# Optimization experiments

Measured on AMD Instinct MI355X. Metric: run time of the kernel, lower is better.

Reference implementation:

```python
import jax, jax.numpy as jnp
import numpy as np

DIM = 512
NUM_HEADS = 16
WIN = (7, 7)
SIZE = WIN[0] * WIN[1]  # 49
B = 2048   # total windows
NW = 4     # windows per image (mask groups)


def _relative_position_index():
    coords_h = np.arange(WIN[0])
    coords_w = np.arange(WIN[1])
    coords = np.stack(np.meshgrid(coords_h, coords_w, indexing='ij'))  # [2,Wh,Ww]
    flat = coords.reshape(2, -1)                                       # [2,S]
    rel = flat[:, :, None] - flat[:, None, :]                          # [2,S,S]
    rel = rel.transpose(1, 2, 0)                                       # [S,S,2]
    rel[:, :, 0] += WIN[0] - 1
    rel[:, :, 1] += WIN[1] - 1
    rel[:, :, 0] *= 2 * WIN[1] - 1
    return rel.sum(-1).astype(np.int32)                                # [S,S]


def setup_inputs() -> dict:
    key = jax.random.key(0)
    ks = jax.random.split(key, 8)
    num_bias = (2 * WIN[0] - 1) * (2 * WIN[1] - 1)  # 169
    sd = 1.0 / np.sqrt(DIM)
    return {
        'x': jax.random.normal(ks[0], (B, SIZE, DIM), dtype=jnp.float32),
        'mask': jax.random.normal(ks[1], (NW, SIZE, SIZE), dtype=jnp.float32),
        'w_qkv': jax.random.normal(ks[2], (DIM, 3 * DIM), dtype=jnp.float32) * sd,
        'b_qkv': jnp.zeros((3 * DIM,), dtype=jnp.float32),
        'w_proj': jax.random.normal(ks[3], (DIM, DIM), dtype=jnp.float32) * sd,
        'b_proj': jnp.zeros((DIM,), dtype=jnp.float32),
        'bias_table': jax.random.normal(ks[4], (num_bias, NUM_HEADS), dtype=jnp.float32) * 0.02,
        'rel_idx': jnp.asarray(_relative_position_index()),
    }


def reference(x, mask, w_qkv, b_qkv, w_proj, b_proj, bias_table, rel_idx):
    b, s, c = x.shape
    h = NUM_HEADS
    hd = c // h
    scale = hd ** (-0.5)
    # qkv projection -> [3, B, H, S, hd]
    qkv = (x @ w_qkv + b_qkv).reshape(b, s, 3, h, hd).transpose(2, 0, 3, 1, 4)
    q, k, v = qkv[0] * scale, qkv[1], qkv[2]
    attn = jnp.einsum('bhqd,bhkd->bhqk', q, k)                 # [B,H,S,S]
    # gathered relative position bias -> [H,S,S]
    bias = bias_table[rel_idx.reshape(-1)].reshape(s, s, h).transpose(2, 0, 1)
    attn = attn + bias[None]
    nw = mask.shape[0]
    attn = attn.reshape(b // nw, nw, h, s, s) + mask[None, :, None]
    attn = jax.nn.softmax(attn.reshape(b, h, s, s), axis=-1)
    out = jnp.einsum('bhqk,bhkd->bhqd', attn, v)               # [B,H,S,hd]
    out = out.transpose(0, 2, 1, 3).reshape(b, s, c)
    return out @ w_proj + b_proj
```

## Files before the change

### kernel.cpp

```cpp
#include <hip/hip_runtime.h>
#include <hip/hip_bf16.h>
#include <stdint.h>

typedef float  floatx4 __attribute__((ext_vector_type(4)));
typedef short  short8  __attribute__((ext_vector_type(8)));
typedef unsigned short u16;

#define DIM 512
#define NH 16
#define HD 32
#define WS 49
#define NBW 2048
#define NWIN 4
#define M_TOTAL (NBW*WS)
#define N_QKV (3*DIM)

__device__ __forceinline__ u16 f2bf(float f) {
    uint32_t u = __float_as_uint(f);
    u += 0x7FFFu + ((u >> 16) & 1u);
    return (u16)(u >> 16);
}

__device__ __forceinline__ void load_lds16(const u16* g, u16* l) {
    __builtin_amdgcn_global_load_lds(
        (const __attribute__((address_space(1))) unsigned int*)g,
        (__attribute__((address_space(3))) unsigned int*)l, 16, 0, 0);
}

__global__ void cast_x_kernel(const float* __restrict__ in, u16* __restrict__ out, int n4) {
    int i = blockIdx.x * blockDim.x + threadIdx.x;
    if (i >= n4) return;
    const float4 v = ((const float4*)in)[i];
    ushort4 o;
    o.x = f2bf(v.x); o.y = f2bf(v.y); o.z = f2bf(v.z); o.w = f2bf(v.w);
    ((ushort4*)out)[i] = o;
}

__global__ void transpose_cast_kernel(const float* __restrict__ in, u16* __restrict__ out,
                                      int N, int total) {
    int idx = blockIdx.x * blockDim.x + threadIdx.x;
    if (idx >= total) return;
    int k = idx & (DIM - 1);
    int n = idx >> 9;
    out[idx] = f2bf(in[k * N + n]);
}

__global__ void build_comb_kernel(const float* __restrict__ bias_table, const int* __restrict__ rel_idx,
                                  const float* __restrict__ mask, float* __restrict__ comb) {
    int idx = blockIdx.x * blockDim.x + threadIdx.x;
    if (idx >= NWIN * NH * 64 * 64) return;
    int c = idx & 3, jj = (idx >> 2) & 15, i = (idx >> 6) & 63, h = (idx >> 12) & 15, g = idx >> 16;
    int j = c * 16 + jj;
    float v = -1e30f;
    if (i < WS && j < WS)
        v = bias_table[rel_idx[i * WS + j] * NH + h] + mask[(g * WS + i) * WS + j];
    comb[idx] = v;
}

template<bool OUT_BF16>
__global__ __launch_bounds__(256, 2) void gemm_bt_kernel(
    const u16* __restrict__ A, const u16* __restrict__ Bt,
    const float* __restrict__ bias, void* __restrict__ out, int N, int K)
{
    __shared__ __align__(16) u16 sA[128 * 32];
    __shared__ __align__(16) u16 sB[128 * 32];
    const int tid  = threadIdx.x;
    const int lane = tid & 63;
    const int wave = tid >> 6;
    const long m0 = (long)blockIdx.y * 128;
    const long n0 = (long)blockIdx.x * 128;
    const int rr = lane & 15;
    const int qk = (lane >> 4) * 8;
    const int wm = (wave >> 1) * 64;
    const int wn = (wave & 1) * 64;

    floatx4 acc[4][4];
    const floatx4 z4 = {0.f, 0.f, 0.f, 0.f};
#pragma unroll
    for (int mi = 0; mi < 4; ++mi)
#pragma unroll
        for (int ni = 0; ni < 4; ++ni) acc[mi][ni] = z4;

    const int row0 = tid >> 2;
    const int kc0  = (tid & 3) * 8;
    const u16* gA0 = A  + (m0 + row0) * K + kc0;
    const u16* gA1 = A  + (m0 + row0 + 64) * K + kc0;
    const u16* gB0 = Bt + (n0 + row0) * K + kc0;
    const u16* gB1 = Bt + (n0 + row0 + 64) * K + kc0;
    u16* lA0 = sA + tid * 8;
    u16* lA1 = sA + (tid + 256) * 8;
    u16* lB0 = sB + tid * 8;
    u16* lB1 = sB + (tid + 256) * 8;

    for (int k0 = 0; k0 < K; k0 += 32) {
        load_lds16(gA0 + k0, lA0);
        load_lds16(gA1 + k0, lA1);
        load_lds16(gB0 + k0, lB0);
        load_lds16(gB1 + k0, lB1);
        __syncthreads();
        short8 af[4], bfr[4];
#pragma unroll
        for (int mi = 0; mi < 4; ++mi)
            af[mi] = *(const short8*)(sA + (wm + mi * 16 + rr) * 32 + qk);
#pragma unroll
        for (int ni = 0; ni < 4; ++ni)
            bfr[ni] = *(const short8*)(sB + (wn + ni * 16 + rr) * 32 + qk);
#pragma unroll
        for (int mi = 0; mi < 4; ++mi)
#pragma unroll
            for (int ni = 0; ni < 4; ++ni)
                acc[mi][ni] = __builtin_amdgcn_mfma_f32_16x16x32_bf16(af[mi], bfr[ni], acc[mi][ni], 0, 0, 0);
        __syncthreads();
    }

#pragma unroll
    for (int mi = 0; mi < 4; ++mi) {
#pragma unroll
        for (int r = 0; r < 4; ++r) {
            const long m = m0 + wm + mi * 16 + (lane >> 4) * 4 + r;
#pragma unroll
            for (int ni = 0; ni < 4; ++ni) {
                const long n = n0 + wn + ni * 16 + rr;
                float v = acc[mi][ni][r] + bias[n];
                if (OUT_BF16) ((u16*)out)[m * N + n] = f2bf(v);
                else          ((float*)out)[m * N + n] = v;
            }
        }
    }
}

__global__ __launch_bounds__(256, 4) void attn_kernel(
    const u16* __restrict__ qkv, const float* __restrict__ comb,
    u16* __restrict__ attn_out)
{
    const int w   = threadIdx.x >> 6;
    const int l   = threadIdx.x & 63;
    const int job = blockIdx.x * 4 + w;
    const int b    = job >> 5;
    const int h    = (job >> 1) & 15;
    const int half = job & 1;
    const int row0 = half * 32;
    const int rr = l & 15;
    const int q4 = l >> 4;
    const int qk = q4 * 8;

    __shared__ __align__(16) u16 p_s[4][32 * 64];
    u16* ps = p_s[w];

    const u16* qg = qkv + (long)b * WS * N_QKV + h * HD;
    const u16* kg = qg + DIM;
    const u16* vg = qg + 2 * DIM;

    const short8 z8 = {0, 0, 0, 0, 0, 0, 0, 0};
    const floatx4 z4 = {0.f, 0.f, 0.f, 0.f};

    short8 af[2], bfr[4];
#pragma unroll
    for (int mi = 0; mi < 2; ++mi) {
        const int row = row0 + mi * 16 + rr;
        af[mi] = (row < WS) ? *(const short8*)(qg + (long)row * N_QKV + qk) : z8;
    }
#pragma unroll
    for (int ni = 0; ni < 4; ++ni) {
        const int row = ni * 16 + rr;
        bfr[ni] = (row < WS) ? *(const short8*)(kg + (long)row * N_QKV + qk) : z8;
    }

    short8 vf[2][2];
#pragma unroll
    for (int kk = 0; kk < 2; ++kk)
#pragma unroll
        for (int ni = 0; ni < 2; ++ni) {
            short8 t = z8;
            const int d = 2 * rr + ni;
#pragma unroll
            for (int j = 0; j < 8; ++j) {
                const int s = kk * 32 + qk + j;
                if (s < WS) t[j] = (short)vg[(long)s * N_QKV + d];
            }
            vf[kk][ni] = t;
        }
    short8 vones;
#pragma unroll
    for (int j = 0; j < 8; ++j) vones[j] = (short)0x3F80;

    floatx4 sc[2][4];
#pragma unroll
    for (int mi = 0; mi < 2; ++mi)
#pragma unroll
        for (int ni = 0; ni < 4; ++ni)
            sc[mi][ni] = __builtin_amdgcn_mfma_f32_16x16x32_bf16(af[mi], bfr[ni], z4, 0, 0, 0);

    const float4* cb4 = (const float4*)comb + ((long)((b & (NWIN - 1)) * NH + h)) * 1024;
    const float scale = 0.17677669529663689f;
#pragma unroll
    for (int mi = 0; mi < 2; ++mi) {
#pragma unroll
        for (int r = 0; r < 4; ++r) {
            const int il = mi * 16 + q4 * 4 + r;
            const float4 cb = cb4[(row0 + il) * 16 + rr];
            float e0 = __expf(sc[mi][0][r] * scale + cb.x);
            float e1 = __expf(sc[mi][1][r] * scale + cb.y);
            float e2 = __expf(sc[mi][2][r] * scale + cb.z);
            float e3 = __expf(sc[mi][3][r] * scale + cb.w);
#pragma unroll
            for (int c = 0; c < 4; ++c) {
                const int col = c * 16 + rr;
                const int blk = (col >> 3) ^ (il & 7);
                const float ev = (c == 0) ? e0 : (c == 1) ? e1 : (c == 2) ? e2 : e3;
                ps[il * 64 + blk * 8 + (col & 7)] = f2bf(ev);
            }
        }
    }
    asm volatile("s_waitcnt lgkmcnt(0)" ::: "memory");

    floatx4 oacc[2][3];
#pragma unroll
    for (int mi = 0; mi < 2; ++mi) { oacc[mi][0] = z4; oacc[mi][1] = z4; oacc[mi][2] = z4; }
#pragma unroll
    for (int kk = 0; kk < 2; ++kk) {
        short8 pf[2];
#pragma unroll
        for (int mi = 0; mi < 2; ++mi) {
            const int i2 = mi * 16 + rr;
            pf[mi] = *(const short8*)(ps + i2 * 64 + (((4 * kk + q4) ^ (i2 & 7)) * 8));
        }
#pragma unroll
        for (int mi = 0; mi < 2; ++mi) {
            oacc[mi][0] = __builtin_amdgcn_mfma_f32_16x16x32_bf16(pf[mi], vf[kk][0], oacc[mi][0], 0, 0, 0);
            oacc[mi][1] = __builtin_amdgcn_mfma_f32_16x16x32_bf16(pf[mi], vf[kk][1], oacc[mi][1], 0, 0, 0);
            oacc[mi][2] = __builtin_amdgcn_mfma_f32_16x16x32_bf16(pf[mi], vones,     oacc[mi][2], 0, 0, 0);
        }
    }

#pragma unroll
    for (int mi = 0; mi < 2; ++mi) {
#pragma unroll
        for (int r = 0; r < 4; ++r) {
            const int ig = row0 + mi * 16 + q4 * 4 + r;
            if (ig < WS) {
                const float inv = 1.0f / oacc[mi][2][r];
                const uint32_t lo = f2bf(oacc[mi][0][r] * inv);
                const uint32_t hi = f2bf(oacc[mi][1][r] * inv);
                uint32_t* op = (uint32_t*)(attn_out + ((long)(b * WS + ig)) * DIM + h * HD);
                op[rr] = lo | (hi << 16);
            }
        }
    }
}

extern "C" void kernel_launch(void* const* d_in, const int* in_sizes, int n_in,
                              void* d_out, int out_size, void* d_ws, size_t ws_size,
                              hipStream_t stream)
{
    const float* x          = (const float*)d_in[0];
    const float* mask       = (const float*)d_in[1];
    const float* w_qkv      = (const float*)d_in[2];
    const float* b_qkv      = (const float*)d_in[3];
    const float* w_proj     = (const float*)d_in[4];
    const float* b_proj     = (const float*)d_in[5];
    const float* bias_table = (const float*)d_in[6];
    const int*   rel_idx    = (const int*)d_in[7];
    float* out = (float*)d_out;

    char* ws = (char*)d_ws;
    u16* x_bf   = (u16*)ws;  ws += (size_t)M_TOTAL * DIM * 2;
    u16* wqkvT  = (u16*)ws;  ws += (size_t)N_QKV * DIM * 2;
    u16* wprojT = (u16*)ws;  ws += (size_t)DIM * DIM * 2;
    float* comb = (float*)ws; ws += (size_t)NWIN * NH * 64 * 64 * 4;
    u16* qkv    = (u16*)ws;  ws += (size_t)M_TOTAL * N_QKV * 2;
    u16* attn_o = x_bf;

    const int n4 = M_TOTAL * DIM / 4;
    cast_x_kernel<<<(n4 + 255) / 256, 256, 0, stream>>>(x, x_bf, n4);
    transpose_cast_kernel<<<(N_QKV * DIM + 255) / 256, 256, 0, stream>>>(w_qkv, wqkvT, N_QKV, N_QKV * DIM);
    transpose_cast_kernel<<<(DIM * DIM + 255) / 256, 256, 0, stream>>>(w_proj, wprojT, DIM, DIM * DIM);
    build_comb_kernel<<<(NWIN * NH * 64 * 64 + 255) / 256, 256, 0, stream>>>(bias_table, rel_idx, mask, comb);

    gemm_bt_kernel<true><<<dim3(N_QKV / 128, M_TOTAL / 128), 256, 0, stream>>>(
        x_bf, wqkvT, b_qkv, qkv, N_QKV, DIM);

    attn_kernel<<<NBW * NH * 2 / 4, 256, 0, stream>>>(qkv, comb, attn_o);

    gemm_bt_kernel<false><<<dim3(DIM / 128, M_TOTAL / 128), 256, 0, stream>>>(
        attn_o, wprojT, b_proj, out, DIM, DIM);
}
```

Before: 856.7 us.

## Swizzle GEMM LDS and block order, tile weight transpose, merge attention halves

Several independent changes land together. The weight transpose-cast now goes through a padded shared-memory tile so both the reads and the writes are coalesced. The GEMM XOR-swizzles its LDS columns to cut bank conflicts on fragment reads, and remaps block IDs into groups of eight to improve L2 locality. The attention kernel now has each wave handle all 64 query rows of a head instead of 32, so K and V fragments are loaded once per head rather than twice. This doubles per-wave LDS and register use and halves the number of attention waves.

Result: faster. 784.3 us (-8.5%).

```diff
diff --git a/kernel.cpp b/kernel.cpp
--- a/kernel.cpp
+++ b/kernel.cpp
@@ -36,13 +36,19 @@
     ((ushort4*)out)[i] = o;
 }
 
-__global__ void transpose_cast_kernel(const float* __restrict__ in, u16* __restrict__ out,
-                                      int N, int total) {
-    int idx = blockIdx.x * blockDim.x + threadIdx.x;
-    if (idx >= total) return;
-    int k = idx & (DIM - 1);
-    int n = idx >> 9;
-    out[idx] = f2bf(in[k * N + n]);
+__global__ void transpose_cast_kernel(const float* __restrict__ in, u16* __restrict__ out, int N) {
+    __shared__ float t[32][33];
+    const int bx = blockIdx.x * 32;
+    const int by = blockIdx.y * 32;
+    const int lx = threadIdx.x & 31;
+    const int ly = threadIdx.x >> 5;
+#pragma unroll
+    for (int i = 0; i < 32; i += 8)
+        t[ly + i][lx] = in[(long)(by + ly + i) * N + bx + lx];
+    __syncthreads();
+#pragma unroll
+    for (int i = 0; i < 32; i += 8)
+        out[(long)(bx + ly + i) * 512 + by + lx] = f2bf(t[lx][ly + i]);
 }
 
 __global__ void build_comb_kernel(const float* __restrict__ bias_table, const int* __restrict__ rel_idx,
@@ -67,10 +73,17 @@
     const int tid  = threadIdx.x;
     const int lane = tid & 63;
     const int wave = tid >> 6;
-    const long m0 = (long)blockIdx.y * 128;
-    const long n0 = (long)blockIdx.x * 128;
+
+    const int GXd = gridDim.x;
+    const int nwg = GXd * gridDim.y;
+    int fb = blockIdx.y * GXd + blockIdx.x;
+    fb = (fb & 7) * (nwg >> 3) + (fb >> 3);
+    const long m0 = (long)(fb / GXd) * 128;
+    const long n0 = (long)(fb % GXd) * 128;
+
     const int rr = lane & 15;
-    const int qk = (lane >> 4) * 8;
+    const int rq = lane >> 4;
+    const int cs = (rq ^ ((lane >> 1) & 3)) * 8;
     const int wm = (wave >> 1) * 64;
     const int wn = (wave & 1) * 64;
 
@@ -82,11 +95,11 @@
         for (int ni = 0; ni < 4; ++ni) acc[mi][ni] = z4;
 
     const int row0 = tid >> 2;
-    const int kc0  = (tid & 3) * 8;
-    const u16* gA0 = A  + (m0 + row0) * K + kc0;
-    const u16* gA1 = A  + (m0 + row0 + 64) * K + kc0;
-    const u16* gB0 = Bt + (n0 + row0) * K + kc0;
-    const u16* gB1 = Bt + (n0 + row0 + 64) * K + kc0;
+    const int ssw  = ((tid & 3) ^ ((tid >> 3) & 3)) * 8;
+    const u16* gA0 = A  + (m0 + row0) * K + ssw;
+    const u16* gA1 = A  + (m0 + row0 + 64) * K + ssw;
+    const u16* gB0 = Bt + (n0 + row0) * K + ssw;
+    const u16* gB1 = Bt + (n0 + row0 + 64) * K + ssw;
     u16* lA0 = sA + tid * 8;
     u16* lA1 = sA + (tid + 256) * 8;
     u16* lB0 = sB + tid * 8;
@@ -101,10 +114,10 @@
         short8 af[4], bfr[4];
 #pragma unroll
         for (int mi = 0; mi < 4; ++mi)
-            af[mi] = *(const short8*)(sA + (wm + mi * 16 + rr) * 32 + qk);
+            af[mi] = *(const short8*)(sA + (wm + mi * 16 + rr) * 32 + cs);
 #pragma unroll
         for (int ni = 0; ni < 4; ++ni)
-            bfr[ni] = *(const short8*)(sB + (wn + ni * 16 + rr) * 32 + qk);
+            bfr[ni] = *(const short8*)(sB + (wn + ni * 16 + rr) * 32 + cs);
 #pragma unroll
         for (int mi = 0; mi < 4; ++mi)
 #pragma unroll
@@ -117,7 +130,7 @@
     for (int mi = 0; mi < 4; ++mi) {
 #pragma unroll
         for (int r = 0; r < 4; ++r) {
-            const long m = m0 + wm + mi * 16 + (lane >> 4) * 4 + r;
+            const long m = m0 + wm + mi * 16 + rq * 4 + r;
 #pragma unroll
             for (int ni = 0; ni < 4; ++ni) {
                 const long n = n0 + wn + ni * 16 + rr;
@@ -136,15 +149,13 @@
     const int w   = threadIdx.x >> 6;
     const int l   = threadIdx.x & 63;
     const int job = blockIdx.x * 4 + w;
-    const int b    = job >> 5;
-    const int h    = (job >> 1) & 15;
-    const int half = job & 1;
-    const int row0 = half * 32;
+    const int b   = job >> 4;
+    const int h   = job & 15;
     const int rr = l & 15;
     const int q4 = l >> 4;
     const int qk = q4 * 8;
 
-    __shared__ __align__(16) u16 p_s[4][32 * 64];
+    __shared__ __align__(16) u16 p_s[4][64 * 64];
     u16* ps = p_s[w];
 
     const u16* qg = qkv + (long)b * WS * N_QKV + h * HD;
@@ -154,12 +165,7 @@
     const short8 z8 = {0, 0, 0, 0, 0, 0, 0, 0};
     const floatx4 z4 = {0.f, 0.f, 0.f, 0.f};
 
-    short8 af[2], bfr[4];
-#pragma unroll
-    for (int mi = 0; mi < 2; ++mi) {
-        const int row = row0 + mi * 16 + rr;
-        af[mi] = (row < WS) ? *(const short8*)(qg + (long)row * N_QKV + qk) : z8;
-    }
+    short8 bfr[4];
 #pragma unroll
     for (int ni = 0; ni < 4; ++ni) {
         const int row = ni * 16 + rr;
@@ -184,25 +190,30 @@
 #pragma unroll
     for (int j = 0; j < 8; ++j) vones[j] = (short)0x3F80;
 
-    floatx4 sc[2][4];
-#pragma unroll
-    for (int mi = 0; mi < 2; ++mi)
-#pragma unroll
-        for (int ni = 0; ni < 4; ++ni)
-            sc[mi][ni] = __builtin_amdgcn_mfma_f32_16x16x32_bf16(af[mi], bfr[ni], z4, 0, 0, 0);
+    short8 af[4];
+#pragma unroll
+    for (int mi = 0; mi < 4; ++mi) {
+        const int row = mi * 16 + rr;
+        af[mi] = (row < WS) ? *(const short8*)(qg + (long)row * N_QKV + qk) : z8;
+    }
 
     const float4* cb4 = (const float4*)comb + ((long)((b & (NWIN - 1)) * NH + h)) * 1024;
     const float scale = 0.17677669529663689f;
-#pragma unroll
-    for (int mi = 0; mi < 2; ++mi) {
+
+#pragma unroll
+    for (int mi = 0; mi < 4; ++mi) {
+        floatx4 scm[4];
+#pragma unroll
+        for (int ni = 0; ni < 4; ++ni)
+            scm[ni] = __builtin_amdgcn_mfma_f32_16x16x32_bf16(af[mi], bfr[ni], z4, 0, 0, 0);
 #pragma unroll
         for (int r = 0; r < 4; ++r) {
             const int il = mi * 16 + q4 * 4 + r;
-            const float4 cb = cb4[(row0 + il) * 16 + rr];
-            float e0 = __expf(sc[mi][0][r] * scale + cb.x);
-            float e1 = __expf(sc[mi][1][r] * scale + cb.y);
-            float e2 = __expf(sc[mi][2][r] * scale + cb.z);
-            float e3 = __expf(sc[mi][3][r] * scale + cb.w);
+            const float4 cb = cb4[il * 16 + rr];
+            float e0 = __expf(scm[0][r] * scale + cb.x);
+            float e1 = __expf(scm[1][r] * scale + cb.y);
+            float e2 = __expf(scm[2][r] * scale + cb.z);
+            float e3 = __expf(scm[3][r] * scale + cb.w);
 #pragma unroll
             for (int c = 0; c < 4; ++c) {
                 const int col = c * 16 + rr;
@@ -214,19 +225,19 @@
     }
     asm volatile("s_waitcnt lgkmcnt(0)" ::: "memory");
 
-    floatx4 oacc[2][3];
-#pragma unroll
-    for (int mi = 0; mi < 2; ++mi) { oacc[mi][0] = z4; oacc[mi][1] = z4; oacc[mi][2] = z4; }
+    floatx4 oacc[4][3];
+#pragma unroll
+    for (int mi = 0; mi < 4; ++mi) { oacc[mi][0] = z4; oacc[mi][1] = z4; oacc[mi][2] = z4; }
 #pragma unroll
     for (int kk = 0; kk < 2; ++kk) {
-        short8 pf[2];
-#pragma unroll
-        for (int mi = 0; mi < 2; ++mi) {
+        short8 pf[4];
+#pragma unroll
+        for (int mi = 0; mi < 4; ++mi) {
             const int i2 = mi * 16 + rr;
             pf[mi] = *(const short8*)(ps + i2 * 64 + (((4 * kk + q4) ^ (i2 & 7)) * 8));
         }
 #pragma unroll
-        for (int mi = 0; mi < 2; ++mi) {
+        for (int mi = 0; mi < 4; ++mi) {
             oacc[mi][0] = __builtin_amdgcn_mfma_f32_16x16x32_bf16(pf[mi], vf[kk][0], oacc[mi][0], 0, 0, 0);
             oacc[mi][1] = __builtin_amdgcn_mfma_f32_16x16x32_bf16(pf[mi], vf[kk][1], oacc[mi][1], 0, 0, 0);
             oacc[mi][2] = __builtin_amdgcn_mfma_f32_16x16x32_bf16(pf[mi], vones,     oacc[mi][2], 0, 0, 0);
@@ -234,10 +245,10 @@
     }
 
 #pragma unroll
-    for (int mi = 0; mi < 2; ++mi) {
+    for (int mi = 0; mi < 4; ++mi) {
 #pragma unroll
         for (int r = 0; r < 4; ++r) {
-            const int ig = row0 + mi * 16 + q4 * 4 + r;
+            const int ig = mi * 16 + q4 * 4 + r;
             if (ig < WS) {
                 const float inv = 1.0f / oacc[mi][2][r];
                 const uint32_t lo = f2bf(oacc[mi][0][r] * inv);
@@ -273,14 +284,14 @@
 
     const int n4 = M_TOTAL * DIM / 4;
     cast_x_kernel<<<(n4 + 255) / 256, 256, 0, stream>>>(x, x_bf, n4);
-    transpose_cast_kernel<<<(N_QKV * DIM + 255) / 256, 256, 0, stream>>>(w_qkv, wqkvT, N_QKV, N_QKV * DIM);
-    transpose_cast_kernel<<<(DIM * DIM + 255) / 256, 256, 0, stream>>>(w_proj, wprojT, DIM, DIM * DIM);
+    transpose_cast_kernel<<<dim3(N_QKV / 32, 16), 256, 0, stream>>>(w_qkv, wqkvT, N_QKV);
+    transpose_cast_kernel<<<dim3(DIM / 32, 16), 256, 0, stream>>>(w_proj, wprojT, DIM);
     build_comb_kernel<<<(NWIN * NH * 64 * 64 + 255) / 256, 256, 0, stream>>>(bias_table, rel_idx, mask, comb);
 
     gemm_bt_kernel<true><<<dim3(N_QKV / 128, M_TOTAL / 128), 256, 0, stream>>>(
         x_bf, wqkvT, b_qkv, qkv, N_QKV, DIM);
 
-    attn_kernel<<<NBW * NH * 2 / 4, 256, 0, stream>>>(qkv, comb, attn_o);
+    attn_kernel<<<NBW * NH / 4, 256, 0, stream>>>(qkv, comb, attn_o);
 
     gemm_bt_kernel<false><<<dim3(DIM / 128, M_TOTAL / 128), 256, 0, stream>>>(
         attn_o, wprojT, b_proj, out, DIM, DIM);
```
